# Kernel tuning notes

Measured on AMD Instinct MI355X. Metric: run time of the kernel, lower is better.

## Reference

```python
import jax, jax.numpy as jnp
import numpy as np
import math

BLKQ = 64
BLKK = 32
TOPK_FRAC = 0.1


def setup_inputs() -> dict:
    key = jax.random.key(0)
    k1, k2, k3, k4, k5 = jax.random.split(key, 5)
    B, L, H, D = 1, 8192, 16, 64
    q = jax.random.normal(k1, (B, L, H, D), jnp.float32)
    k = jax.random.normal(k2, (B, L, H, D), jnp.float32)
    v = jax.random.normal(k3, (B, L, H, D), jnp.float32)
    # proj_l initialized with nn.init.normal_ (std=1) in the original
    W_proj = jax.random.normal(k4, (D, D), jnp.float32)
    b_proj = jax.random.normal(k5, (D,), jnp.float32)
    return {"q": q, "k": k, "v": v, "W_proj": W_proj, "b_proj": b_proj}


def reference(q, k, v, W_proj, b_proj):
    B, L, H, D = q.shape
    lcm = BLKQ * BLKK // math.gcd(BLKQ, BLKK)
    L_pad = ((L + lcm - 1) // lcm) * lcm
    pad = L_pad - L
    scale = 1.0 / math.sqrt(D)

    # [B, L, H, D] -> [B, H, L_pad, D], zero padded (fused_transpose_pad)
    qt = jnp.transpose(q, (0, 2, 1, 3))
    kt = jnp.transpose(k, (0, 2, 1, 3))
    vt = jnp.transpose(v, (0, 2, 1, 3))
    if pad:
        pw = ((0, 0), (0, 0), (0, pad), (0, 0))
        qt_p = jnp.pad(qt, pw); kt_p = jnp.pad(kt, pw); vt_p = jnp.pad(vt, pw)
    else:
        qt_p, kt_p, vt_p = qt, kt, vt

    # key smoothing (SAGE): subtract per-(b,h) mean of padded k
    km = kt_p.mean(axis=-2, keepdims=True)          # [B, H, 1, D]
    kc = kt_p - km

    M = L_pad // BLKQ
    N = L_pad // BLKK
    # block pooling for routing scores
    pooled_q = qt_p.reshape(B, H, M, BLKQ, D).mean(axis=3)   # [B,H,M,D]
    pooled_k = kc.reshape(B, H, N, BLKK, D).mean(axis=3)     # [B,H,N,D]
    score = jnp.einsum('bhmd,bhnd->bhmn', pooled_q, pooled_k)

    T = min(N, int(TOPK_FRAC * N))                  # real_topk (static)
    _, idx = jax.lax.top_k(score, T)                # [B,H,M,T]
    lut = jnp.sort(idx, axis=-1)

    # gather selected key/value blocks: [B,H,M,T,BLKK,D]
    kb = kc.reshape(B, H, N, BLKK, D)
    vb = vt_p.reshape(B, H, N, BLKK, D)
    kg = jnp.take_along_axis(kb[:, :, None], lut[..., None, None], axis=3)
    vg = jnp.take_along_axis(vb[:, :, None], lut[..., None, None], axis=3)

    qb = qt_p.reshape(B, H, M, BLKQ, D)
    # block-sparse scores: [B,H,M,BLKQ,T,BLKK]
    s = jnp.einsum('bhmqd,bhmtkd->bhmqtk', qb, kg) * scale
    key_pos = lut[..., None] * BLKK + jnp.arange(BLKK)       # [B,H,M,T,BLKK]
    valid = key_pos < L
    s = jnp.where(valid[:, :, :, None, :, :], s, -jnp.inf)
    s = s.reshape(B, H, M, BLKQ, T * BLKK)
    p = jax.nn.softmax(s, axis=-1)
    o_s = jnp.einsum('bhmqn,bhmnd->bhmqd', p, vg.reshape(B, H, M, T * BLKK, D))
    o_s = o_s.reshape(B, H, L_pad, D)[:, :, :L]              # slice to seq_len

    # linear attention branch (softmax feature map over D)
    q_fm = jax.nn.softmax(qt_p[:, :, :L], axis=-1)
    k_fm = jax.nn.softmax(kt_p[:, :, :L], axis=-1)
    kvsum = jnp.einsum('bhld,bhle->bhde', k_fm, vt)          # [B,H,D,D]
    ksum = k_fm.sum(axis=-2)                                 # [B,H,D]
    denom = jnp.einsum('bhld,bhd->bhl', q_fm, ksum)[..., None] + 1e-6
    o_l = jnp.einsum('bhld,bhde->bhle', q_fm, kvsum) / denom
    o_l = o_l @ W_proj.T + b_proj                            # proj_l

    o = jnp.transpose(o_l + o_s, (0, 2, 1, 3))               # [B,L,H,D]
    return o
```

## Files before the change

kernel.cpp:

```cpp
#include <hip/hip_runtime.h>
#include <math.h>

#define SEQL 8192
#define NH 16
#define HD 1024
#define TSEL 25

#define OFF_KVPART 0
#define OFF_KSUM   262144
#define OFF_ZEND   263168
#define OFF_PK     263168
#define OFF_KWT    525312
#define OFF_KSWZ   558080
#define OFF_PQ     0
#define OFF_LUT    131072

typedef __attribute__((ext_vector_type(8))) short bf16x8;
typedef __attribute__((ext_vector_type(4))) float f32x4;

static __device__ inline short f2bf(float f) {
    union { float f; unsigned u; } c; c.f = f;
    unsigned r = (c.u + 0x7FFFu + ((c.u >> 16) & 1u)) >> 16;
    return (short)r;
}
static __device__ inline bf16x8 cvt8(float4 a, float4 b) {
    bf16x8 r;
    r[0] = f2bf(a.x); r[1] = f2bf(a.y); r[2] = f2bf(a.z); r[3] = f2bf(a.w);
    r[4] = f2bf(b.x); r[5] = f2bf(b.y); r[6] = f2bf(b.z); r[7] = f2bf(b.w);
    return r;
}
static __device__ inline unsigned cvtpk(float a, float b) {
    unsigned r;
    asm("v_cvt_pk_bf16_f32 %0, %1, %2" : "=v"(r) : "v"(a), "v"(b));
    return r;
}
static __device__ inline float exp2a(float x) {
#if __has_builtin(__builtin_amdgcn_exp2f)
    return __builtin_amdgcn_exp2f(x);
#else
    float r; asm("v_exp_f32 %0, %1" : "=v"(r) : "v"(x)); return r;
#endif
}
static __device__ inline void load_lds16(const void* g, void* l) {
    __builtin_amdgcn_global_load_lds((const __attribute__((address_space(1))) unsigned int*)g,
                                     (__attribute__((address_space(3))) unsigned int*)l,
                                     16, 0, 0);
}

__global__ __launch_bounds__(256) void prep_kv(const float* __restrict__ k,
                                               const float* __restrict__ v,
                                               short* __restrict__ kswz,
                                               short* __restrict__ vswz,
                                               float* __restrict__ pk) {
    __shared__ float pcol[4][64];
    int b = blockIdx.x;
    int h = b >> 8, n = b & 255;
    int t = threadIdx.x;
    {
        int r = t >> 3, ch = t & 7;
        const float* src = k + (size_t)(n * 32 + r) * HD + h * 64 + ch * 8;
        float4 f0 = *(const float4*)src, f1 = *(const float4*)(src + 4);
        int f = r * 8 + (ch ^ (r & 7));
        *(bf16x8*)(kswz + (size_t)b * 2048 + f * 8) = cvt8(f0, f1);
        float s[8] = { f0.x, f0.y, f0.z, f0.w, f1.x, f1.y, f1.z, f1.w };
        #pragma unroll
        for (int j = 0; j < 8; j++) {
            s[j] += __shfl_xor(s[j], 8, 64);
            s[j] += __shfl_xor(s[j], 16, 64);
            s[j] += __shfl_xor(s[j], 32, 64);
        }
        if ((t & 63) < 8) {
            #pragma unroll
            for (int j = 0; j < 8; j++) pcol[t >> 6][(t & 7) * 8 + j] = s[j];
        }
    }
    {
        int c = t >> 6, d = t & 63;
        const float* src = v + (size_t)(n * 32 + c * 8) * HD + h * 64 + d;
        bf16x8 val;
        #pragma unroll
        for (int j = 0; j < 8; j++) val[j] = f2bf(src[(size_t)j * HD]);
        int f = d * 4 + (c ^ ((d >> 1) & 3));
        *(bf16x8*)(vswz + (size_t)b * 2048 + f * 8) = val;
    }
    __syncthreads();
    if (t < 64)
        pk[(size_t)b * 64 + t] =
            (pcol[0][t] + pcol[1][t] + pcol[2][t] + pcol[3][t]) * (1.f / 32.f);
}

__global__ void pool_q(const float* __restrict__ q, float* __restrict__ pq) {
    int b = blockIdx.x;
    int h = b >> 7, m = b & 127, d = threadIdx.x;
    const float* base = q + (size_t)m * 64 * HD + h * 64 + d;
    float s = 0.f;
    #pragma unroll 8
    for (int r = 0; r < 64; r++) s += base[(size_t)r * HD];
    pq[(size_t)b * 64 + d] = s * (1.f / 64.f);
}

__global__ __launch_bounds__(256) void score_topk(const float* __restrict__ pq,
                                                  const float* __restrict__ pk,
                                                  int* __restrict__ lut) {
    __shared__ __align__(16) float pq_s[64];
    __shared__ __align__(16) float s_s[256];
    __shared__ int wcnt[4];
    int b = blockIdx.x;
    int h = b >> 7;
    int t = threadIdx.x;
    int lane = t & 63, w = t >> 6;
    if (t < 64) pq_s[t] = pq[(size_t)b * 64 + t];
    __syncthreads();
    const float* kr = pk + ((size_t)h * 256 + t) * 64;
    double acc = 0.0;
    #pragma unroll 8
    for (int d = 0; d < 64; d++) acc += (double)pq_s[d] * (double)kr[d];
    float sc = (float)acc;
    s_s[t] = sc;
    __syncthreads();
    int cnt = 0;
    float si = sc;
    #pragma unroll 4
    for (int j4 = 0; j4 < 64; j4++) {
        float4 sv = *(const float4*)&s_s[j4 * 4];
        int j = j4 * 4;
        cnt += (sv.x > si) || (sv.x == si && (j + 0) < t);
        cnt += (sv.y > si) || (sv.y == si && (j + 1) < t);
        cnt += (sv.z > si) || (sv.z == si && (j + 2) < t);
        cnt += (sv.w > si) || (sv.w == si && (j + 3) < t);
    }
    bool sel = cnt < TSEL;
    unsigned long long bal = __ballot(sel);
    if (lane == 0) wcnt[w] = __popcll(bal);
    __syncthreads();
    if (sel) {
        int off = __popcll(bal & ((1ull << lane) - 1ull));
        for (int i = 0; i < w; i++) off += wcnt[i];
        lut[(size_t)b * TSEL + off] = t;
    }
}

__global__ __launch_bounds__(256) void lin_kv(const float* __restrict__ k,
                                              const float* __restrict__ v,
                                              float* __restrict__ kvpart,
                                              float* __restrict__ ksum) {
    __shared__ __align__(16) float kf[32][66];
    __shared__ __align__(16) float vv[32][66];
    int b = blockIdx.x;
    int h = b >> 6, c0 = b & 63;
    int t = threadIdx.x;
    int lane = t & 63, w = t >> 6;
    int prow = t >> 3, c8 = (t & 7) * 8;
    int d0 = (lane & 15) * 4, e0 = (lane >> 4) * 4 + w * 16;
    float acc[16];
    #pragma unroll
    for (int i = 0; i < 16; i++) acc[i] = 0.f;
    float ks_acc = 0.f;
    for (int half = 0; half < 4; half++) {
        int lr = (c0 + (half >> 1) * 64) * 64 + (half & 1) * 32;
        const float* ksrc = k + (size_t)(lr + prow) * HD + h * 64 + c8;
        const float* vsrc = v + (size_t)(lr + prow) * HD + h * 64 + c8;
        float4 X0 = *(const float4*)ksrc;
        float4 X1 = *(const float4*)(ksrc + 4);
        float4 V0 = *(const float4*)vsrc;
        float4 V1 = *(const float4*)(vsrc + 4);
        *(float4*)&vv[prow][c8] = V0;
        *(float4*)&vv[prow][c8 + 4] = V1;
        float mx = fmaxf(fmaxf(fmaxf(X0.x, X0.y), fmaxf(X0.z, X0.w)),
                         fmaxf(fmaxf(X1.x, X1.y), fmaxf(X1.z, X1.w)));
        mx = fmaxf(mx, __shfl_xor(mx, 1, 64));
        mx = fmaxf(mx, __shfl_xor(mx, 2, 64));
        mx = fmaxf(mx, __shfl_xor(mx, 4, 64));
        X0.x = __expf(X0.x - mx); X0.y = __expf(X0.y - mx);
        X0.z = __expf(X0.z - mx); X0.w = __expf(X0.w - mx);
        X1.x = __expf(X1.x - mx); X1.y = __expf(X1.y - mx);
        X1.z = __expf(X1.z - mx); X1.w = __expf(X1.w - mx);
        float sm = (X0.x + X0.y + X0.z + X0.w) + (X1.x + X1.y + X1.z + X1.w);
        sm += __shfl_xor(sm, 1, 64);
        sm += __shfl_xor(sm, 2, 64);
        sm += __shfl_xor(sm, 4, 64);
        float inv = 1.f / sm;
        X0.x *= inv; X0.y *= inv; X0.z *= inv; X0.w *= inv;
        X1.x *= inv; X1.y *= inv; X1.z *= inv; X1.w *= inv;
        *(float4*)&kf[prow][c8] = X0;
        *(float4*)&kf[prow][c8 + 4] = X1;
        __syncthreads();
        #pragma unroll 8
        for (int l = 0; l < 32; l++) {
            float4 kd = *(const float4*)&kf[l][d0];
            float4 ve = *(const float4*)&vv[l][e0];
            acc[0]  += kd.x * ve.x; acc[1]  += kd.x * ve.y; acc[2]  += kd.x * ve.z; acc[3]  += kd.x * ve.w;
            acc[4]  += kd.y * ve.x; acc[5]  += kd.y * ve.y; acc[6]  += kd.y * ve.z; acc[7]  += kd.y * ve.w;
            acc[8]  += kd.z * ve.x; acc[9]  += kd.z * ve.y; acc[10] += kd.z * ve.z; acc[11] += kd.z * ve.w;
            acc[12] += kd.w * ve.x; acc[13] += kd.w * ve.y; acc[14] += kd.w * ve.z; acc[15] += kd.w * ve.w;
        }
        if (t < 64) {
            float s = 0.f;
            #pragma unroll 8
            for (int l = 0; l < 32; l++) s += kf[l][t];
            ks_acc += s;
        }
        __syncthreads();
    }
    float* dst = kvpart + ((size_t)(b & 3) * 16 + h) * 4096;
    #pragma unroll
    for (int i = 0; i < 4; i++)
        #pragma unroll
        for (int j = 0; j < 4; j++)
            atomicAdd(&dst[(d0 + i) * 64 + e0 + j], acc[i * 4 + j]);
    if (t < 64) atomicAdd(&ksum[h * 64 + t], ks_acc);
}

__global__ __launch_bounds__(256) void kw_mul(const float* __restrict__ kvpart,
                                              const float* __restrict__ W,
                                              short* __restrict__ kwt) {
    __shared__ __align__(16) float kv[16][68];
    __shared__ __align__(16) float wsm[64][68];
    int h = blockIdx.x >> 2, dq = blockIdx.x & 3;
    int t = threadIdx.x;
    for (int i = t; i < 1024; i += 256) {
        int dl = i >> 6, e = i & 63;
        float s = 0.f;
        #pragma unroll
        for (int p = 0; p < 4; p++)
            s += kvpart[((size_t)p * 16 + h) * 4096 + (dq * 16 + dl) * 64 + e];
        kv[dl][e] = s;
    }
    for (int i = t; i < 4096; i += 256) wsm[i >> 6][i & 63] = W[i];
    __syncthreads();
    int lane = t & 63, wi = t >> 6;
    int dl = lane & 15;
    int db = wi * 16 + (lane >> 4) * 4;
    #pragma unroll
    for (int j = 0; j < 4; j++) {
        int dd = db + j;
        float a = 0.f;
        #pragma unroll
        for (int e4 = 0; e4 < 16; e4++) {
            float4 kq = *(const float4*)&kv[dl][e4 * 4];
            float4 wq = *(const float4*)&wsm[dd][e4 * 4];
            a += kq.x * wq.x + kq.y * wq.y + kq.z * wq.z + kq.w * wq.w;
        }
        kwt[(size_t)h * 4096 + dd * 64 + dq * 16 + dl] = f2bf(a);
    }
}

__global__ __launch_bounds__(256) void sparse_attn_mfma(const float* __restrict__ q,
                                                        const short* __restrict__ kswz,
                                                        const short* __restrict__ vswz,
                                                        const int* __restrict__ lut,
                                                        const short* __restrict__ kwt,
                                                        const float* __restrict__ ksum,
                                                        const float* __restrict__ bproj,
                                                        float* __restrict__ out) {
    __shared__ __align__(16) short Kb[2][2048];
    __shared__ __align__(16) short Vb[2][2048];
    __shared__ __align__(16) short Pl[64][40];
    __shared__ int lut_s[TSEL];

    int b = blockIdx.x;
    int x = b & 7, jj = b >> 3;
    int h = x * 2 + (jj >> 7);
    int m = jj & 127;
    int t = threadIdx.x;
    int lane = t & 63, w = t >> 6;
    int l15 = lane & 15, quad = lane >> 4;

    if (t < TSEL) lut_s[t] = lut[(size_t)(h * 128 + m) * TSEL + t];
    __syncthreads();

    {
        size_t base = (size_t)(h * 256 + lut_s[0]) * 2048;
        load_lds16(kswz + base + t * 8, &Kb[0][t * 8]);
        load_lds16(vswz + base + t * 8, &Vb[0][t * 8]);
        load_lds16(kwt + (size_t)h * 4096 + t * 8, &Kb[1][t * 8]);
        load_lds16(kwt + (size_t)h * 4096 + 2048 + t * 8, &Vb[1][t * 8]);
    }

    const float* qrow = q + (size_t)(m * 64 + w * 16 + l15) * HD + h * 64;
    float4 x0 = *(const float4*)(qrow + quad * 8);
    float4 x1 = *(const float4*)(qrow + quad * 8 + 4);
    float4 x2 = *(const float4*)(qrow + 32 + quad * 8);
    float4 x3 = *(const float4*)(qrow + 32 + quad * 8 + 4);
    bf16x8 qa[2];
    qa[0] = cvt8(x0, x1);
    qa[1] = cvt8(x2, x3);

    float mx = fmaxf(fmaxf(fmaxf(x0.x, x0.y), fmaxf(x0.z, x0.w)),
                     fmaxf(fmaxf(x1.x, x1.y), fmaxf(x1.z, x1.w)));
    mx = fmaxf(mx, fmaxf(fmaxf(fmaxf(x2.x, x2.y), fmaxf(x2.z, x2.w)),
                         fmaxf(fmaxf(x3.x, x3.y), fmaxf(x3.z, x3.w))));
    mx = fmaxf(mx, __shfl_xor(mx, 16, 64));
    mx = fmaxf(mx, __shfl_xor(mx, 32, 64));
    x0.x = __expf(x0.x - mx); x0.y = __expf(x0.y - mx); x0.z = __expf(x0.z - mx); x0.w = __expf(x0.w - mx);
    x1.x = __expf(x1.x - mx); x1.y = __expf(x1.y - mx); x1.z = __expf(x1.z - mx); x1.w = __expf(x1.w - mx);
    x2.x = __expf(x2.x - mx); x2.y = __expf(x2.y - mx); x2.z = __expf(x2.z - mx); x2.w = __expf(x2.w - mx);
    x3.x = __expf(x3.x - mx); x3.y = __expf(x3.y - mx); x3.z = __expf(x3.z - mx); x3.w = __expf(x3.w - mx);
    float sm = (x0.x + x0.y + x0.z + x0.w) + (x1.x + x1.y + x1.z + x1.w)
             + (x2.x + x2.y + x2.z + x2.w) + (x3.x + x3.y + x3.z + x3.w);
    sm += __shfl_xor(sm, 16, 64);
    sm += __shfl_xor(sm, 32, 64);
    float qsc = 1.f / sm;
    float4 ka0 = *(const float4*)(ksum + h * 64 + quad * 8);
    float4 ka1 = *(const float4*)(ksum + h * 64 + quad * 8 + 4);
    float4 ka2 = *(const float4*)(ksum + h * 64 + 32 + quad * 8);
    float4 ka3 = *(const float4*)(ksum + h * 64 + 32 + quad * 8 + 4);
    float dq = x0.x * ka0.x + x0.y * ka0.y + x0.z * ka0.z + x0.w * ka0.w
             + x1.x * ka1.x + x1.y * ka1.y + x1.z * ka1.z + x1.w * ka1.w
             + x2.x * ka2.x + x2.y * ka2.y + x2.z * ka2.z + x2.w * ka2.w
             + x3.x * ka3.x + x3.y * ka3.y + x3.z * ka3.z + x3.w * ka3.w;
    dq += __shfl_xor(dq, 16, 64);
    dq += __shfl_xor(dq, 32, 64);
    float invd = 1.f / (dq * qsc + 1e-6f);
    x0.x *= qsc; x0.y *= qsc; x0.z *= qsc; x0.w *= qsc;
    x1.x *= qsc; x1.y *= qsc; x1.z *= qsc; x1.w *= qsc;
    x2.x *= qsc; x2.y *= qsc; x2.z *= qsc; x2.w *= qsc;
    x3.x *= qsc; x3.y *= qsc; x3.z *= qsc; x3.w *= qsc;
    bf16x8 qf[2];
    qf[0] = cvt8(x0, x1);
    qf[1] = cvt8(x2, x3);

    __syncthreads();

    f32x4 Ol[4];
    #pragma unroll
    for (int dt = 0; dt < 4; dt++) Ol[dt] = (f32x4){0.f, 0.f, 0.f, 0.f};
    __builtin_amdgcn_s_setprio(1);
    #pragma unroll
    for (int dt = 0; dt < 4; dt++) {
        #pragma unroll
        for (int kc = 0; kc < 2; kc++) {
            int flat = (dt * 16 + l15) * 64 + kc * 32 + quad * 8;
            bf16x8 a = (dt < 2) ? *(const bf16x8*)&Kb[1][flat]
                                : *(const bf16x8*)&Vb[1][flat - 2048];
            Ol[dt] = __builtin_amdgcn_mfma_f32_16x16x32_bf16(a, qf[kc], Ol[dt], 0, 0, 0);
        }
    }
    __builtin_amdgcn_s_setprio(0);

    f32x4 O[4];
    #pragma unroll
    for (int dt = 0; dt < 4; dt++) O[dt] = (f32x4){0.f, 0.f, 0.f, 0.f};
    float l_i = 0.f;
    const f32x4 z = (f32x4){0.f, 0.f, 0.f, 0.f};
    const float EC = 1.44269504f * 0.125f;

    for (int ti = 0; ti < TSEL; ti++) {
        __syncthreads();
        int buf = ti & 1;
        if (ti + 1 < TSEL) {
            size_t base = (size_t)(h * 256 + lut_s[ti + 1]) * 2048;
            load_lds16(kswz + base + t * 8, &Kb[buf ^ 1][t * 8]);
            load_lds16(vswz + base + t * 8, &Vb[buf ^ 1][t * 8]);
        }
        int r0 = l15, r1 = 16 + l15;
        bf16x8 a00 = *(const bf16x8*)&Kb[buf][(r0 * 8 + (quad ^ (r0 & 7))) * 8];
        bf16x8 a01 = *(const bf16x8*)&Kb[buf][(r0 * 8 + ((4 + quad) ^ (r0 & 7))) * 8];
        bf16x8 a10 = *(const bf16x8*)&Kb[buf][(r1 * 8 + (quad ^ (r1 & 7))) * 8];
        bf16x8 a11 = *(const bf16x8*)&Kb[buf][(r1 * 8 + ((4 + quad) ^ (r1 & 7))) * 8];
        __builtin_amdgcn_s_setprio(1);
        f32x4 s0 = __builtin_amdgcn_mfma_f32_16x16x32_bf16(a00, qa[0], z, 0, 0, 0);
        s0 = __builtin_amdgcn_mfma_f32_16x16x32_bf16(a01, qa[1], s0, 0, 0, 0);
        f32x4 s1 = __builtin_amdgcn_mfma_f32_16x16x32_bf16(a10, qa[0], z, 0, 0, 0);
        s1 = __builtin_amdgcn_mfma_f32_16x16x32_bf16(a11, qa[1], s1, 0, 0, 0);
        __builtin_amdgcn_s_setprio(0);

        float p0[4], p1[4];
        float lsum = 0.f;
        #pragma unroll
        for (int r = 0; r < 4; r++) {
            p0[r] = exp2a(s0[r] * EC);
            p1[r] = exp2a(s1[r] * EC);
            lsum += p0[r] + p1[r];
        }
        lsum += __shfl_xor(lsum, 16, 64);
        lsum += __shfl_xor(lsum, 32, 64);
        l_i += lsum;

        uint2 pkA, pkB;
        pkA.x = cvtpk(p0[0], p0[1]); pkA.y = cvtpk(p0[2], p0[3]);
        pkB.x = cvtpk(p1[0], p1[1]); pkB.y = cvtpk(p1[2], p1[3]);
        *(uint2*)&Pl[w * 16 + l15][quad * 4] = pkA;
        *(uint2*)&Pl[w * 16 + l15][16 + quad * 4] = pkB;

        asm volatile("s_waitcnt lgkmcnt(0)\n\ts_barrier" ::: "memory");

        bf16x8 pb = *(const bf16x8*)&Pl[w * 16 + l15][quad * 8];
        __builtin_amdgcn_s_setprio(1);
        #pragma unroll
        for (int dt = 0; dt < 4; dt++) {
            int d = dt * 16 + l15;
            bf16x8 va = *(const bf16x8*)&Vb[buf][(d * 4 + (quad ^ ((d >> 1) & 3))) * 8];
            O[dt] = __builtin_amdgcn_mfma_f32_16x16x32_bf16(va, pb, O[dt], 0, 0, 0);
        }
        __builtin_amdgcn_s_setprio(0);
    }

    float inv = 1.f / l_i;
    float* dst = out + (size_t)(m * 64 + w * 16 + l15) * HD + h * 64;
    #pragma unroll
    for (int dt = 0; dt < 4; dt++) {
        float4 bv = *(const float4*)(bproj + dt * 16 + quad * 4);
        float4 o;
        o.x = O[dt][0] * inv + Ol[dt][0] * invd + bv.x;
        o.y = O[dt][1] * inv + Ol[dt][1] * invd + bv.y;
        o.z = O[dt][2] * inv + Ol[dt][2] * invd + bv.z;
        o.w = O[dt][3] * inv + Ol[dt][3] * invd + bv.w;
        *(float4*)(dst + dt * 16 + quad * 4) = o;
    }
}

extern "C" void kernel_launch(void* const* d_in, const int* in_sizes, int n_in,
                              void* d_out, int out_size, void* d_ws, size_t ws_size,
                              hipStream_t stream) {
    const float* q  = (const float*)d_in[0];
    const float* k  = (const float*)d_in[1];
    const float* v  = (const float*)d_in[2];
    const float* W  = (const float*)d_in[3];
    const float* bp = (const float*)d_in[4];
    float* out = (float*)d_out;
    float* ws = (float*)d_ws;

    float* kvpart = ws + OFF_KVPART;
    float* ksum   = ws + OFF_KSUM;
    float* pk     = ws + OFF_PK;
    short* kwt    = (short*)(ws + OFF_KWT);
    short* kswz   = (short*)(ws + OFF_KSWZ);
    short* vswz   = kswz + (size_t)16 * 256 * 2048;
    float* pq     = ws + OFF_PQ;
    int*   lut    = (int*)(ws + OFF_LUT);

    hipMemsetAsync(ws, 0, OFF_ZEND * sizeof(float), stream);
    prep_kv<<<4096, 256, 0, stream>>>(k, v, kswz, vswz, pk);
    lin_kv<<<1024, 256, 0, stream>>>(k, v, kvpart, ksum);
    kw_mul<<<64, 256, 0, stream>>>(kvpart, W, kwt);
    pool_q<<<2048, 64, 0, stream>>>(q, pq);
    score_topk<<<2048, 256, 0, stream>>>(pq, pk, lut);
    sparse_attn_mfma<<<2048, 256, 0, stream>>>(q, kswz, vswz, lut, kwt, ksum, bp, out);
}
```

Baseline: 314.8 us.

## Fuse query pooling into score_topk and restructure lin_kv to one 64-row chunk per block

Removes the separate pool_q kernel by computing each block's pooled query inside score_topk, which saves a launch and the pq round trip through global memory. lin_kv now processes a single 64-row chunk per block with 2048 blocks instead of looping over four 32-row chunks in 1024 blocks. Each thread loads 16 contiguous floats, and the block needs only one sync before the outer-product accumulation. The trade-off is twice as many atomicAdds to kvpart and ksum, plus larger shared tiles.

```diff
diff --git a/kernel.cpp b/kernel.cpp
--- a/kernel.cpp
+++ b/kernel.cpp
@@ -12,7 +12,6 @@
 #define OFF_PK     263168
 #define OFF_KWT    525312
 #define OFF_KSWZ   558080
-#define OFF_PQ     0
 #define OFF_LUT    131072
 
 typedef __attribute__((ext_vector_type(8))) short bf16x8;
@@ -89,27 +88,23 @@
             (pcol[0][t] + pcol[1][t] + pcol[2][t] + pcol[3][t]) * (1.f / 32.f);
 }
 
-__global__ void pool_q(const float* __restrict__ q, float* __restrict__ pq) {
-    int b = blockIdx.x;
-    int h = b >> 7, m = b & 127, d = threadIdx.x;
-    const float* base = q + (size_t)m * 64 * HD + h * 64 + d;
-    float s = 0.f;
-    #pragma unroll 8
-    for (int r = 0; r < 64; r++) s += base[(size_t)r * HD];
-    pq[(size_t)b * 64 + d] = s * (1.f / 64.f);
-}
-
-__global__ __launch_bounds__(256) void score_topk(const float* __restrict__ pq,
+__global__ __launch_bounds__(256) void score_topk(const float* __restrict__ q,
                                                   const float* __restrict__ pk,
                                                   int* __restrict__ lut) {
     __shared__ __align__(16) float pq_s[64];
     __shared__ __align__(16) float s_s[256];
     __shared__ int wcnt[4];
     int b = blockIdx.x;
-    int h = b >> 7;
+    int h = b >> 7, m = b & 127;
     int t = threadIdx.x;
     int lane = t & 63, w = t >> 6;
-    if (t < 64) pq_s[t] = pq[(size_t)b * 64 + t];
+    if (t < 64) {
+        const float* base = q + (size_t)m * 64 * HD + h * 64 + t;
+        float s = 0.f;
+        #pragma unroll 8
+        for (int r = 0; r < 64; r++) s += base[(size_t)r * HD];
+        pq_s[t] = s * (1.f / 64.f);
+    }
     __syncthreads();
     const float* kr = pk + ((size_t)h * 256 + t) * 64;
     double acc = 0.0;
@@ -144,71 +139,72 @@
                                               const float* __restrict__ v,
                                               float* __restrict__ kvpart,
                                               float* __restrict__ ksum) {
-    __shared__ __align__(16) float kf[32][66];
-    __shared__ __align__(16) float vv[32][66];
+    __shared__ __align__(16) float kf[64][68];
+    __shared__ __align__(16) float vv[64][68];
     int b = blockIdx.x;
-    int h = b >> 6, c0 = b & 63;
+    int h = b >> 7, chunk = b & 127;
+    int l0 = chunk * 64;
     int t = threadIdx.x;
     int lane = t & 63, w = t >> 6;
-    int prow = t >> 3, c8 = (t & 7) * 8;
-    int d0 = (lane & 15) * 4, e0 = (lane >> 4) * 4 + w * 16;
+    int row = t >> 2, c16 = (t & 3) * 16;
+    const float4* ks4 = (const float4*)(k + (size_t)(l0 + row) * HD + h * 64 + c16);
+    const float4* vs4 = (const float4*)(v + (size_t)(l0 + row) * HD + h * 64 + c16);
+    {
+        float4* vd = (float4*)&vv[row][c16];
+        #pragma unroll
+        for (int i = 0; i < 4; i++) vd[i] = vs4[i];
+    }
+    float4 X0 = ks4[0], X1 = ks4[1], X2 = ks4[2], X3 = ks4[3];
+    float mx = fmaxf(fmaxf(fmaxf(X0.x, X0.y), fmaxf(X0.z, X0.w)),
+                     fmaxf(fmaxf(X1.x, X1.y), fmaxf(X1.z, X1.w)));
+    mx = fmaxf(mx, fmaxf(fmaxf(fmaxf(X2.x, X2.y), fmaxf(X2.z, X2.w)),
+                         fmaxf(fmaxf(X3.x, X3.y), fmaxf(X3.z, X3.w))));
+    mx = fmaxf(mx, __shfl_xor(mx, 1, 64));
+    mx = fmaxf(mx, __shfl_xor(mx, 2, 64));
+    X0.x = __expf(X0.x - mx); X0.y = __expf(X0.y - mx); X0.z = __expf(X0.z - mx); X0.w = __expf(X0.w - mx);
+    X1.x = __expf(X1.x - mx); X1.y = __expf(X1.y - mx); X1.z = __expf(X1.z - mx); X1.w = __expf(X1.w - mx);
+    X2.x = __expf(X2.x - mx); X2.y = __expf(X2.y - mx); X2.z = __expf(X2.z - mx); X2.w = __expf(X2.w - mx);
+    X3.x = __expf(X3.x - mx); X3.y = __expf(X3.y - mx); X3.z = __expf(X3.z - mx); X3.w = __expf(X3.w - mx);
+    float sm = (X0.x + X0.y + X0.z + X0.w) + (X1.x + X1.y + X1.z + X1.w)
+             + (X2.x + X2.y + X2.z + X2.w) + (X3.x + X3.y + X3.z + X3.w);
+    sm += __shfl_xor(sm, 1, 64);
+    sm += __shfl_xor(sm, 2, 64);
+    float inv = 1.f / sm;
+    X0.x *= inv; X0.y *= inv; X0.z *= inv; X0.w *= inv;
+    X1.x *= inv; X1.y *= inv; X1.z *= inv; X1.w *= inv;
+    X2.x *= inv; X2.y *= inv; X2.z *= inv; X2.w *= inv;
+    X3.x *= inv; X3.y *= inv; X3.z *= inv; X3.w *= inv;
+    {
+        float4* kd = (float4*)&kf[row][c16];
+        kd[0] = X0; kd[1] = X1; kd[2] = X2; kd[3] = X3;
+    }
+    __syncthreads();
+    int d0 = (lane & 15) * 4;
+    int e0 = ((lane >> 4) + w * 4) * 4;
     float acc[16];
     #pragma unroll
     for (int i = 0; i < 16; i++) acc[i] = 0.f;
-    float ks_acc = 0.f;
-    for (int half = 0; half < 4; half++) {
-        int lr = (c0 + (half >> 1) * 64) * 64 + (half & 1) * 32;
-        const float* ksrc = k + (size_t)(lr + prow) * HD + h * 64 + c8;
-        const float* vsrc = v + (size_t)(lr + prow) * HD + h * 64 + c8;
-        float4 X0 = *(const float4*)ksrc;
-        float4 X1 = *(const float4*)(ksrc + 4);
-        float4 V0 = *(const float4*)vsrc;
-        float4 V1 = *(const float4*)(vsrc + 4);
-        *(float4*)&vv[prow][c8] = V0;
-        *(float4*)&vv[prow][c8 + 4] = V1;
-        float mx = fmaxf(fmaxf(fmaxf(X0.x, X0.y), fmaxf(X0.z, X0.w)),
-                         fmaxf(fmaxf(X1.x, X1.y), fmaxf(X1.z, X1.w)));
-        mx = fmaxf(mx, __shfl_xor(mx, 1, 64));
-        mx = fmaxf(mx, __shfl_xor(mx, 2, 64));
-        mx = fmaxf(mx, __shfl_xor(mx, 4, 64));
-        X0.x = __expf(X0.x - mx); X0.y = __expf(X0.y - mx);
-        X0.z = __expf(X0.z - mx); X0.w = __expf(X0.w - mx);
-        X1.x = __expf(X1.x - mx); X1.y = __expf(X1.y - mx);
-        X1.z = __expf(X1.z - mx); X1.w = __expf(X1.w - mx);
-        float sm = (X0.x + X0.y + X0.z + X0.w) + (X1.x + X1.y + X1.z + X1.w);
-        sm += __shfl_xor(sm, 1, 64);
-        sm += __shfl_xor(sm, 2, 64);
-        sm += __shfl_xor(sm, 4, 64);
-        float inv = 1.f / sm;
-        X0.x *= inv; X0.y *= inv; X0.z *= inv; X0.w *= inv;
-        X1.x *= inv; X1.y *= inv; X1.z *= inv; X1.w *= inv;
-        *(float4*)&kf[prow][c8] = X0;
-        *(float4*)&kf[prow][c8 + 4] = X1;
-        __syncthreads();
-        #pragma unroll 8
-        for (int l = 0; l < 32; l++) {
-            float4 kd = *(const float4*)&kf[l][d0];
-            float4 ve = *(const float4*)&vv[l][e0];
-            acc[0]  += kd.x * ve.x; acc[1]  += kd.x * ve.y; acc[2]  += kd.x * ve.z; acc[3]  += kd.x * ve.w;
-            acc[4]  += kd.y * ve.x; acc[5]  += kd.y * ve.y; acc[6]  += kd.y * ve.z; acc[7]  += kd.y * ve.w;
-            acc[8]  += kd.z * ve.x; acc[9]  += kd.z * ve.y; acc[10] += kd.z * ve.z; acc[11] += kd.z * ve.w;
-            acc[12] += kd.w * ve.x; acc[13] += kd.w * ve.y; acc[14] += kd.w * ve.z; acc[15] += kd.w * ve.w;
-        }
-        if (t < 64) {
-            float s = 0.f;
-            #pragma unroll 8
-            for (int l = 0; l < 32; l++) s += kf[l][t];
-            ks_acc += s;
-        }
-        __syncthreads();
-    }
-    float* dst = kvpart + ((size_t)(b & 3) * 16 + h) * 4096;
+    #pragma unroll 8
+    for (int l = 0; l < 64; l++) {
+        float4 kd = *(const float4*)&kf[l][d0];
+        float4 ve = *(const float4*)&vv[l][e0];
+        acc[0]  += kd.x * ve.x; acc[1]  += kd.x * ve.y; acc[2]  += kd.x * ve.z; acc[3]  += kd.x * ve.w;
+        acc[4]  += kd.y * ve.x; acc[5]  += kd.y * ve.y; acc[6]  += kd.y * ve.z; acc[7]  += kd.y * ve.w;
+        acc[8]  += kd.z * ve.x; acc[9]  += kd.z * ve.y; acc[10] += kd.z * ve.z; acc[11] += kd.z * ve.w;
+        acc[12] += kd.w * ve.x; acc[13] += kd.w * ve.y; acc[14] += kd.w * ve.z; acc[15] += kd.w * ve.w;
+    }
+    float* dst = kvpart + ((size_t)(chunk & 3) * 16 + h) * 4096;
     #pragma unroll
     for (int i = 0; i < 4; i++)
         #pragma unroll
         for (int j = 0; j < 4; j++)
             atomicAdd(&dst[(d0 + i) * 64 + e0 + j], acc[i * 4 + j]);
-    if (t < 64) atomicAdd(&ksum[h * 64 + t], ks_acc);
+    if (t < 64) {
+        float s = 0.f;
+        #pragma unroll 8
+        for (int l = 0; l < 64; l++) s += kf[l][t];
+        atomicAdd(&ksum[h * 64 + t], s);
+    }
 }
 
 __global__ __launch_bounds__(256) void kw_mul(const float* __restrict__ kvpart,
@@ -427,14 +423,12 @@
     short* kwt    = (short*)(ws + OFF_KWT);
     short* kswz   = (short*)(ws + OFF_KSWZ);
     short* vswz   = kswz + (size_t)16 * 256 * 2048;
-    float* pq     = ws + OFF_PQ;
     int*   lut    = (int*)(ws + OFF_LUT);
 
     hipMemsetAsync(ws, 0, OFF_ZEND * sizeof(float), stream);
     prep_kv<<<4096, 256, 0, stream>>>(k, v, kswz, vswz, pk);
-    lin_kv<<<1024, 256, 0, stream>>>(k, v, kvpart, ksum);
+    lin_kv<<<2048, 256, 0, stream>>>(k, v, kvpart, ksum);
     kw_mul<<<64, 256, 0, stream>>>(kvpart, W, kwt);
-    pool_q<<<2048, 64, 0, stream>>>(q, pq);
-    score_topk<<<2048, 256, 0, stream>>>(pq, pk, lut);
+    score_topk<<<2048, 256, 0, stream>>>(q, pk, lut);
     sparse_attn_mfma<<<2048, 256, 0, stream>>>(q, kswz, vswz, lut, kwt, ksum, bp, out);
 }
```

After: 358.6 us. 1.14x slower.
